# Performance work log

Measured on AMD Instinct MI355X. Metric: run time of the kernel, lower is better.

Reference implementation:

```python
import jax, jax.numpy as jnp
import numpy as np

# alphas = cfg.model.mmd.alphas ** k for k in range(-3, 2), base = 2.0
ALPHAS = tuple(2.0 ** k for k in range(-3, 2))


def _sq_dist(x, y):
    # x: (..., n, c), y: (..., m, c) -> (..., n, m) squared euclidean distance
    xx = jnp.sum(x * x, axis=-1)[..., :, None]
    yy = jnp.sum(y * y, axis=-1)[..., None, :]
    xy = jnp.einsum('...ic,...jc->...ij', x, y)
    return jnp.maximum(xx + yy - 2.0 * xy, 0.0)


def _multi_gauss(d2):
    # sum over alphas of exp(-alpha * dist^2); d2 is already the squared distance
    return sum(jnp.exp(-a * d2) for a in ALPHAS)


def setup_inputs() -> dict:
    key = jax.random.key(0)
    k1, k2, k3, k4 = jax.random.split(key, 4)
    b, ns, nq, ng, nsf, nqf, c = 8, 5, 75, 4, 49, 49, 64
    support_xf = jax.random.normal(k1, (b, ns, ng, nsf, c), dtype=jnp.float32)
    query_xf = jax.random.normal(k2, (b, nq, ng, nqf, c), dtype=jnp.float32)
    beta = jax.random.uniform(k3, (b, nq, ns, ng, nsf), dtype=jnp.float32)
    gamma = jax.random.uniform(k4, (b, nq, ns, ng, nqf), dtype=jnp.float32)
    return {"support_xf": support_xf, "query_xf": query_xf, "beta": beta, "gamma": gamma}


def reference(support_xf, query_xf, beta, gamma):
    # support_xf: (b, ns, ng, nsf, c); query_xf: (b, nq, ng, nqf, c)
    # beta, gamma: (b, nq, ns, ng, nsf/nqf)
    Kss = _multi_gauss(_sq_dist(support_xf, support_xf))   # (b, ns, ng, nsf, nsf)
    Kqq = _multi_gauss(_sq_dist(query_xf, query_xf))       # (b, nq, ng, nqf, nqf)

    # cross squared distances: (b, nq, ns, ng, nsf, nqf)
    s_sq = jnp.sum(support_xf * support_xf, axis=-1)        # (b, ns, ng, nsf)
    q_sq = jnp.sum(query_xf * query_xf, axis=-1)            # (b, nq, ng, nqf)
    sq_dot = jnp.einsum('bsgic,bvgjc->bvsgij', support_xf, query_xf)
    d2_sq = jnp.maximum(
        s_sq[:, None, :, :, :, None] + q_sq[:, :, None, :, None, :] - 2.0 * sq_dot, 0.0)
    Ksq = _multi_gauss(d2_sq)                               # (b, nq, ns, ng, nsf, nqf)

    # beta^T Kss beta  (Kss broadcast over the query axis)
    mmd_s = jnp.einsum('bvsgi,bsgij,bvsgj->bvsg', beta, Kss, beta)
    # gamma^T Kqq gamma (Kqq broadcast over the support axis)
    mmd_q = jnp.einsum('bvsgi,bvgij,bvsgj->bvsg', gamma, Kqq, gamma)
    # beta^T Ksq gamma
    mmd_sq = jnp.einsum('bvsgi,bvsgij,bvsgj->bvsg', beta, Ksq, gamma)

    mmd_dis = mmd_s + mmd_q - 2.0 * mmd_sq                  # (b, nq, ns, ng)
    return jnp.mean(mmd_dis, axis=-1)                       # (b, nq, ns)
```

## Files before the change

### kernel.cpp

```cpp
#include <hip/hip_runtime.h>

#define BB 8
#define NS 5
#define NQ 75
#define NG 4
#define NF 49
#define CDIM 64

#define SUP2 8192
#define NOUT (BB * NQ * NS)
#define NFORM (BB * NG * NS)
#define NCROSS (BB * NQ * NG * 2)

typedef __attribute__((ext_vector_type(8))) short bf16x8;
typedef __attribute__((ext_vector_type(16))) float f32x16;

__device__ __forceinline__ float multi_gauss(float d2) {
    d2 = fmaxf(d2, 0.f);
    float e  = __expf(-0.125f * d2);
    float e2 = e * e, e4 = e2 * e2, e8 = e4 * e4, e16 = e8 * e8;
    return e + e2 + e4 + e8 + e16;
}
__device__ __forceinline__ float multi_gauss2(float arg) {
    float e  = __builtin_amdgcn_exp2f(arg);
    float e2 = e * e, e4 = e2 * e2, e8 = e4 * e4, e16 = e8 * e8;
    return ((e + e2) + (e4 + e8)) + e16;
}
__device__ __forceinline__ unsigned short f2bf(float x) {
    union { float f; unsigned u; } c; c.f = x;
    unsigned r = c.u + 0x7FFFu + ((c.u >> 16) & 1u);
    return (unsigned short)(r >> 16);
}
__device__ __forceinline__ float bf2f(unsigned short h) {
    union { float f; unsigned u; } c; c.u = ((unsigned)h) << 16; return c.f;
}
__device__ __forceinline__ unsigned pack2bf(float x, float y) {
    return (__float_as_uint(x) >> 16) | (__float_as_uint(y) & 0xffff0000u);
}
__device__ __forceinline__ float wred(float x) {
    for (int o = 32; o; o >>= 1) x += __shfl_down(x, o, 64);
    return x;
}

__global__ __launch_bounds__(256) void prep(
    const float* __restrict__ sup,
    unsigned short* __restrict__ whi, float* __restrict__ wssq,
    float* __restrict__ out)
{
    int idx = blockIdx.x * 256 + threadIdx.x;
    if (idx < NOUT) out[idx] = 0.f;

    int row = idx >> 4, c4 = idx & 15;
    int bg = row >> 8, p = row & 255;
    int b = bg >> 2, g = bg & 3;
    int s = p / 49, i = p - s * 49;
    const float* src = (p < 245)
        ? sup + ((size_t)(((b * NS + s) * NG + g) * NF + i)) * CDIM + c4 * 4 : nullptr;

    float4 x = make_float4(0.f, 0.f, 0.f, 0.f);
    if (src) x = *(const float4*)src;
    ushort4 h4;
    h4.x = f2bf(x.x); h4.y = f2bf(x.y); h4.z = f2bf(x.z); h4.w = f2bf(x.w);
    ((ushort4*)whi)[idx] = h4;
    float v2 = x.x * x.x + x.y * x.y + x.z * x.z + x.w * x.w;
    v2 += __shfl_down(v2, 8, 64);
    v2 += __shfl_down(v2, 4, 64);
    v2 += __shfl_down(v2, 2, 64);
    v2 += __shfl_down(v2, 1, 64);
    if ((idx & 15) == 0) wssq[row] = v2;
}

__global__ __launch_bounds__(256, 5) void mmd_main(
    const unsigned short* __restrict__ whi, const float* __restrict__ wssq,
    const float* __restrict__ sup, const float* __restrict__ qry,
    const float* __restrict__ beta, const float* __restrict__ gamma,
    float* __restrict__ out)
{
    __shared__ __align__(16) union {
        struct {
            union {
                unsigned short Q[64 * 72];
                float kq[2 * 32 * 33];
            } qu;
            float ssqQ[64];
            float ssqS[256];
            float sbetaP[256];
            float sgam[NS][64];
            float red_sq[NS], red_qq[NS];
        } c;
        struct {
            unsigned short A[64 * 72];
            unsigned short Bt[32 * 72];
            float fssq[64];
            float red_s[96];
        } f;
    } sm;

    int blk = blockIdx.x;
    int t = threadIdx.x;
    int w = t >> 6, lane = t & 63, lrow = lane & 31, lhalf = lane >> 5;
    const bf16x8* W = (const bf16x8*)whi;
    const float c2  = -0.18033688f;
    const float k2c =  0.36067376f;

    if (blk >= NFORM) {
        int cc = blk - NFORM;
        int h = cc & 1;
        int g = (cc >> 1) & 3;
        int v = (cc >> 3) % NQ;
        int b = cc / (NQ * NG * 2);
        int qc = h * 32;
        int srow0 = (b * NG + g) * 256;

        const int cMTS[4] = {1, 3, 4, 6};
        const int cMTP[4] = {0, 2, 5, 7};
        int mtS = cMTS[w], mtP = cMTP[w];

        for (int u = t; u < 512; u += 256) {
            int row = u >> 3, c8 = u & 7;
            float4 x0 = make_float4(0.f, 0.f, 0.f, 0.f), x1 = x0;
            if (row < NF) {
                const float4* qp = (const float4*)
                    (qry + ((size_t)(((b * NQ + v) * NG + g) * NF + row)) * CDIM + c8 * 8);
                x0 = qp[0]; x1 = qp[1];
            }
            uint4 pk;
            pk.x = pack2bf(x0.x, x0.y);
            pk.y = pack2bf(x0.z, x0.w);
            pk.z = pack2bf(x1.x, x1.y);
            pk.w = pack2bf(x1.z, x1.w);
            *(uint4*)&sm.c.qu.Q[row * 72 + c8 * 8] = pk;
            float v2 = x0.x * x0.x + x0.y * x0.y + x0.z * x0.z + x0.w * x0.w
                     + x1.x * x1.x + x1.y * x1.y + x1.z * x1.z + x1.w * x1.w;
            v2 += __shfl_down(v2, 4, 64);
            v2 += __shfl_down(v2, 2, 64);
            v2 += __shfl_down(v2, 1, 64);
            if ((u & 7) == 0) sm.c.ssqQ[row] = v2;
        }
        {
            int p = t;
            sm.c.ssqS[p] = wssq[srow0 + p];
            int s = p / 49, i = p - s * 49;
            sm.c.sbetaP[p] = (p < 245)
                ? beta[(size_t)(((b * NQ + v) * NS + s) * NG + g) * NF + i] : 0.f;
            for (int u = t; u < NS * 64; u += 256) {
                int s2 = u >> 6, i2 = u & 63;
                sm.c.sgam[s2][i2] = (i2 < NF)
                    ? gamma[(size_t)(((b * NQ + v) * NS + s2) * NG + g) * NF + i2] : 0.f;
            }
            if (t < NS) { sm.c.red_sq[t] = 0.f; sm.c.red_qq[t] = 0.f; }
        }
        __syncthreads();

        f32x16 acc[3];
#pragma unroll
        for (int mi = 0; mi < 3; ++mi)
#pragma unroll
            for (int q = 0; q < 16; ++q) acc[mi][q] = 0.f;

        const unsigned short* Qs = sm.c.qu.Q;
#pragma unroll
        for (int kc = 0; kc < 4; ++kc) {
            int ko = kc * 2 + lhalf;
            int qoff = kc * 16 + lhalf * 8;
            bf16x8 bh = *(const bf16x8*)&Qs[(qc + lrow) * 72 + qoff];
            bf16x8 a0 = W[(srow0 + mtS * 32 + lrow) * 8 + ko];
            bf16x8 a1 = W[(srow0 + mtP * 32 + lrow) * 8 + ko];
            acc[0] = __builtin_amdgcn_mfma_f32_32x32x16_bf16(a0, bh, acc[0], 0, 0, 0);
            acc[1] = __builtin_amdgcn_mfma_f32_32x32x16_bf16(a1, bh, acc[1], 0, 0, 0);
            if (w >= 2) {
                bf16x8 a2 = *(const bf16x8*)&Qs[((w - 2) * 32 + lrow) * 72 + qoff];
                acc[2] = __builtin_amdgcn_mfma_f32_32x32x16_bf16(a2, bh, acc[2], 0, 0, 0);
            }
        }
        __syncthreads();

        if (w >= 2) {
            float* kq = sm.c.qu.kq;
            int base = (w - 2) * 1056 + lrow;
#pragma unroll
            for (int reg = 0; reg < 16; ++reg) {
                int r32 = (reg & 3) + 8 * (reg >> 2) + 4 * lhalf;
                kq[base + r32 * 33] = acc[2][reg];
            }
        }

        float qsq = sm.c.ssqQ[qc + lrow];
        float c2q = c2 * qsq;

        float tsA, tsB;
        {
            int s_lo = (mtS * 32) / 49;
            int bnd = (s_lo + 1) * 49;
            float tA = 0.f, tB = 0.f;
#pragma unroll
            for (int grp = 0; grp < 4; ++grp) {
                int rbase = mtS * 32 + grp * 8 + 4 * lhalf;
                float4 sqv = *(const float4*)&sm.c.ssqS[rbase];
                float4 bvv = *(const float4*)&sm.c.sbetaP[rbase];
#pragma unroll
                for (int q = 0; q < 4; ++q) {
                    float sq = (q == 0) ? sqv.x : (q == 1) ? sqv.y : (q == 2) ? sqv.z : sqv.w;
                    float bv = (q == 0) ? bvv.x : (q == 1) ? bvv.y : (q == 2) ? bvv.z : bvv.w;
                    float arg = fmaf(k2c, acc[0][grp * 4 + q], fmaf(c2, sq, c2q));
                    float con = bv * multi_gauss2(arg);
                    bool lo = (rbase + q) < bnd;
                    tA += lo ? con : 0.f;
                    tB += lo ? 0.f : con;
                }
            }
            tsA = tA; tsB = tB;
        }
        float tsP;
        {
            float tP = 0.f;
#pragma unroll
            for (int grp = 0; grp < 4; ++grp) {
                int rbase = mtP * 32 + grp * 8 + 4 * lhalf;
                float4 sqv = *(const float4*)&sm.c.ssqS[rbase];
                float4 bvv = *(const float4*)&sm.c.sbetaP[rbase];
#pragma unroll
                for (int q = 0; q < 4; ++q) {
                    float sq = (q == 0) ? sqv.x : (q == 1) ? sqv.y : (q == 2) ? sqv.z : sqv.w;
                    float bv = (q == 0) ? bvv.x : (q == 1) ? bvv.y : (q == 2) ? bvv.z : bvv.w;
                    float arg = fmaf(k2c, acc[1][grp * 4 + q], fmaf(c2, sq, c2q));
                    tP = fmaf(bv, multi_gauss2(arg), tP);
                }
            }
            tsP = tP;
        }
        {
            int s_lo = (mtS * 32) / 49;
            int s_hi = s_lo + 1;
            int sP = (mtP * 32) / 49;
            float rA = wred(tsA * sm.c.sgam[s_lo][qc + lrow]);
            float rB = wred(tsB * sm.c.sgam[s_hi][qc + lrow]);
            float rP = wred(tsP * sm.c.sgam[sP][qc + lrow]);
            if (lane == 0) {
                atomicAdd(&sm.c.red_sq[s_lo], rA);
                atomicAdd(&sm.c.red_sq[s_hi], rB);
                atomicAdd(&sm.c.red_sq[sP], rP);
            }
        }
        __syncthreads();

        {
            int colg = qc + lrow;
            const float* kq = sm.c.qu.kq;
            float gq[NS];
#pragma unroll
            for (int s = 0; s < NS; ++s) gq[s] = sm.c.sgam[s][colg];
            float qs[NS] = {0.f, 0.f, 0.f, 0.f, 0.f};
#pragma unroll
            for (int gg = 0; gg < 2; ++gg) {
                int rb = w * 16 + lhalf * 8 + gg * 4;
                float4 sqv = *(const float4*)&sm.c.ssqQ[rb];
                float kvv[4];
#pragma unroll
                for (int q = 0; q < 4; ++q) {
                    int row = rb + q;
                    float dot = kq[(row >> 5) * 1056 + (row & 31) * 33 + lrow];
                    float sq = (q == 0) ? sqv.x : (q == 1) ? sqv.y : (q == 2) ? sqv.z : sqv.w;
                    float arg = fmaf(k2c, dot, fmaf(c2, sq, c2q));
                    kvv[q] = (row == colg) ? 5.0f : multi_gauss2(arg);
                }
#pragma unroll
                for (int s = 0; s < NS; ++s) {
                    float4 gi = *(const float4*)&sm.c.sgam[s][rb];
                    qs[s] = fmaf(gi.x, kvv[0], qs[s]);
                    qs[s] = fmaf(gi.y, kvv[1], qs[s]);
                    qs[s] = fmaf(gi.z, kvv[2], qs[s]);
                    qs[s] = fmaf(gi.w, kvv[3], qs[s]);
                }
            }
#pragma unroll
            for (int s = 0; s < NS; ++s) {
                float r = wred(qs[s] * gq[s]);
                if (lane == 0) atomicAdd(&sm.c.red_qq[s], r);
            }
        }
        __syncthreads();
        if (t < NS)
            atomicAdd(&out[((size_t)b * NQ + v) * NS + t],
                      0.25f * sm.c.red_qq[t] - 0.5f * sm.c.red_sq[t]);
    } else {
        int k = blk;
        int s = k % NS;
        int bg = k / NS;
        int g = bg & 3, b = bg >> 2;

        if (t < 96) sm.f.red_s[t] = 0.f;

        for (int u = t; u < 1024; u += 256) {
            int i = u >> 4, c4 = u & 15;
            float4 x = make_float4(0.f, 0.f, 0.f, 0.f);
            if (i < NF)
                x = *(const float4*)(sup + ((size_t)(((b * NS + s) * NG + g) * NF + i)) * CDIM + c4 * 4);
            ushort4 h4;
            h4.x = f2bf(x.x); h4.y = f2bf(x.y); h4.z = f2bf(x.z); h4.w = f2bf(x.w);
            *(ushort4*)&sm.f.A[i * 72 + c4 * 4] = h4;
            float v2 = x.x * x.x + x.y * x.y + x.z * x.z + x.w * x.w;
            v2 += __shfl_down(v2, 8, 64);
            v2 += __shfl_down(v2, 4, 64);
            v2 += __shfl_down(v2, 2, 64);
            v2 += __shfl_down(v2, 1, 64);
            if ((u & 15) == 0) sm.f.fssq[i] = v2;
        }
        __syncthreads();

        int mt = w >> 1, nt = w & 1;
        f32x16 acc;
#pragma unroll
        for (int q = 0; q < 16; ++q) acc[q] = 0.f;
#pragma unroll
        for (int kc = 0; kc < 4; ++kc) {
            int ko = kc * 2 + lhalf;
            bf16x8 a  = *(const bf16x8*)&sm.f.A[(mt * 32 + lrow) * 72 + ko * 8];
            bf16x8 bb = *(const bf16x8*)&sm.f.A[(nt * 32 + lrow) * 72 + ko * 8];
            acc = __builtin_amdgcn_mfma_f32_32x32x16_bf16(a, bb, acc, 0, 0, 0);
        }
        __syncthreads();

        int cj = nt * 32 + lrow;
        float sqj = sm.f.fssq[cj];
#pragma unroll
        for (int reg = 0; reg < 16; ++reg) {
            int ri = mt * 32 + (reg & 3) + 8 * (reg >> 2) + 4 * lhalf;
            float kv = (ri == cj) ? 5.0f : multi_gauss(sm.f.fssq[ri] + sqj - 2.f * acc[reg]);
            sm.f.A[ri * 72 + cj] = f2bf(kv);
        }

        for (int pass = 0; pass < 3; ++pass) {
            __syncthreads();
            for (int u = t; u < 2048; u += 256) {
                int v32 = u >> 6, j = u & 63;
                int v = pass * 32 + v32;
                unsigned short val = 0;
                if (v < NQ && j < NF)
                    val = f2bf(beta[(size_t)(((b * NQ + v) * NS + s) * NG + g) * NF + j]);
                sm.f.Bt[v32 * 72 + j] = val;
            }
            __syncthreads();
            if (w < 2) {
                int m = w;
                f32x16 yacc;
#pragma unroll
                for (int q = 0; q < 16; ++q) yacc[q] = 0.f;
#pragma unroll
                for (int kc = 0; kc < 4; ++kc) {
                    int ko = kc * 2 + lhalf;
                    bf16x8 af = *(const bf16x8*)&sm.f.A[(m * 32 + lrow) * 72 + ko * 8];
                    bf16x8 bf = *(const bf16x8*)&sm.f.Bt[lrow * 72 + ko * 8];
                    yacc = __builtin_amdgcn_mfma_f32_32x32x16_bf16(af, bf, yacc, 0, 0, 0);
                }
                float p = 0.f;
#pragma unroll
                for (int reg = 0; reg < 16; ++reg) {
                    int i = m * 32 + (reg & 3) + 8 * (reg >> 2) + 4 * lhalf;
                    p = fmaf(yacc[reg], bf2f(sm.f.Bt[lrow * 72 + i]), p);
                }
                p += __shfl_xor(p, 32, 64);
                if (lane < 32) atomicAdd(&sm.f.red_s[pass * 32 + lrow], p);
            }
        }
        __syncthreads();
        if (t < NQ)
            atomicAdd(&out[((size_t)b * NQ + t) * NS + s], 0.25f * sm.f.red_s[t]);
    }
}

extern "C" void kernel_launch(void* const* d_in, const int* in_sizes, int n_in,
                              void* d_out, int out_size, void* d_ws, size_t ws_size,
                              hipStream_t stream) {
    const float* sup   = (const float*)d_in[0];
    const float* qry   = (const float*)d_in[1];
    const float* beta  = (const float*)d_in[2];
    const float* gamma = (const float*)d_in[3];
    float* out = (float*)d_out;

    unsigned short* whi = (unsigned short*)d_ws;
    float* wssq = (float*)(whi + (size_t)SUP2 * 64);

    prep<<<(SUP2 * 16) / 256, 256, 0, stream>>>(sup, whi, wssq, out);
    mmd_main<<<NFORM + NCROSS, 256, 0, stream>>>(whi, wssq, sup, qry, beta, gamma, out);
}
```

Before: 120.8 us.

## Merge query-column halves into one 512-thread block per cross tile

Each cross-term block now covers both 32-column halves of the query features, using 512 threads (two groups of four waves) instead of two 256-thread blocks. The query tile, gamma, beta and support norms are loaded into shared memory once per (b,v,g) rather than twice, and the shared Kqq dot buffer doubles to hold both halves. Formation blocks also run at 512 threads, but only four waves do the MFMA and kernel-evaluation work. This cuts redundant global loads and block count, at the cost of larger blocks, a bigger shared footprint and idle waves in the formation path.

```diff
diff --git a/kernel.cpp b/kernel.cpp
--- a/kernel.cpp
+++ b/kernel.cpp
@@ -10,7 +10,7 @@
 #define SUP2 8192
 #define NOUT (BB * NQ * NS)
 #define NFORM (BB * NG * NS)
-#define NCROSS (BB * NQ * NG * 2)
+#define NCROSS (BB * NQ * NG)
 
 typedef __attribute__((ext_vector_type(8))) short bf16x8;
 typedef __attribute__((ext_vector_type(16))) float f32x16;
@@ -70,7 +70,7 @@
     if ((idx & 15) == 0) wssq[row] = v2;
 }
 
-__global__ __launch_bounds__(256, 5) void mmd_main(
+__global__ __launch_bounds__(512, 4) void mmd_main(
     const unsigned short* __restrict__ whi, const float* __restrict__ wssq,
     const float* __restrict__ sup, const float* __restrict__ qry,
     const float* __restrict__ beta, const float* __restrict__ gamma,
@@ -80,7 +80,7 @@
         struct {
             union {
                 unsigned short Q[64 * 72];
-                float kq[2 * 32 * 33];
+                float kq[4 * 32 * 33];
             } qu;
             float ssqQ[64];
             float ssqS[256];
@@ -105,19 +105,19 @@
 
     if (blk >= NFORM) {
         int cc = blk - NFORM;
-        int h = cc & 1;
-        int g = (cc >> 1) & 3;
-        int v = (cc >> 3) % NQ;
-        int b = cc / (NQ * NG * 2);
+        int g = cc & 3;
+        int v = (cc >> 2) % NQ;
+        int b = cc / (NQ * NG);
+        int srow0 = (b * NG + g) * 256;
+        int h = w >> 2, w4 = w & 3;
         int qc = h * 32;
-        int srow0 = (b * NG + g) * 256;
 
         const int cMTS[4] = {1, 3, 4, 6};
         const int cMTP[4] = {0, 2, 5, 7};
-        int mtS = cMTS[w], mtP = cMTP[w];
-
-        for (int u = t; u < 512; u += 256) {
-            int row = u >> 3, c8 = u & 7;
+        int mtS = cMTS[w4], mtP = cMTP[w4];
+
+        {
+            int row = t >> 3, c8 = t & 7;
             float4 x0 = make_float4(0.f, 0.f, 0.f, 0.f), x1 = x0;
             if (row < NF) {
                 const float4* qp = (const float4*)
@@ -135,21 +135,21 @@
             v2 += __shfl_down(v2, 4, 64);
             v2 += __shfl_down(v2, 2, 64);
             v2 += __shfl_down(v2, 1, 64);
-            if ((u & 7) == 0) sm.c.ssqQ[row] = v2;
-        }
-        {
+            if ((t & 7) == 0) sm.c.ssqQ[row] = v2;
+        }
+        if (t < 256) {
             int p = t;
             sm.c.ssqS[p] = wssq[srow0 + p];
             int s = p / 49, i = p - s * 49;
             sm.c.sbetaP[p] = (p < 245)
                 ? beta[(size_t)(((b * NQ + v) * NS + s) * NG + g) * NF + i] : 0.f;
-            for (int u = t; u < NS * 64; u += 256) {
-                int s2 = u >> 6, i2 = u & 63;
-                sm.c.sgam[s2][i2] = (i2 < NF)
-                    ? gamma[(size_t)(((b * NQ + v) * NS + s2) * NG + g) * NF + i2] : 0.f;
-            }
-            if (t < NS) { sm.c.red_sq[t] = 0.f; sm.c.red_qq[t] = 0.f; }
-        }
+        }
+        if (t < NS * 64) {
+            int s2 = t >> 6, i2 = t & 63;
+            sm.c.sgam[s2][i2] = (i2 < NF)
+                ? gamma[(size_t)(((b * NQ + v) * NS + s2) * NG + g) * NF + i2] : 0.f;
+        }
+        if (t < NS) { sm.c.red_sq[t] = 0.f; sm.c.red_qq[t] = 0.f; }
         __syncthreads();
 
         f32x16 acc[3];
@@ -168,16 +168,16 @@
             bf16x8 a1 = W[(srow0 + mtP * 32 + lrow) * 8 + ko];
             acc[0] = __builtin_amdgcn_mfma_f32_32x32x16_bf16(a0, bh, acc[0], 0, 0, 0);
             acc[1] = __builtin_amdgcn_mfma_f32_32x32x16_bf16(a1, bh, acc[1], 0, 0, 0);
-            if (w >= 2) {
-                bf16x8 a2 = *(const bf16x8*)&Qs[((w - 2) * 32 + lrow) * 72 + qoff];
+            if (w4 >= 2) {
+                bf16x8 a2 = *(const bf16x8*)&Qs[((w4 - 2) * 32 + lrow) * 72 + qoff];
                 acc[2] = __builtin_amdgcn_mfma_f32_32x32x16_bf16(a2, bh, acc[2], 0, 0, 0);
             }
         }
         __syncthreads();
 
-        if (w >= 2) {
+        if (w4 >= 2) {
             float* kq = sm.c.qu.kq;
-            int base = (w - 2) * 1056 + lrow;
+            int base = (h * 2 + (w4 - 2)) * 1056 + lrow;
 #pragma unroll
             for (int reg = 0; reg < 16; ++reg) {
                 int r32 = (reg & 3) + 8 * (reg >> 2) + 4 * lhalf;
@@ -253,13 +253,13 @@
             float qs[NS] = {0.f, 0.f, 0.f, 0.f, 0.f};
 #pragma unroll
             for (int gg = 0; gg < 2; ++gg) {
-                int rb = w * 16 + lhalf * 8 + gg * 4;
+                int rb = w4 * 16 + lhalf * 8 + gg * 4;
                 float4 sqv = *(const float4*)&sm.c.ssqQ[rb];
                 float kvv[4];
 #pragma unroll
                 for (int q = 0; q < 4; ++q) {
                     int row = rb + q;
-                    float dot = kq[(row >> 5) * 1056 + (row & 31) * 33 + lrow];
+                    float dot = kq[(h * 2 + (row >> 5)) * 1056 + (row & 31) * 33 + lrow];
                     float sq = (q == 0) ? sqv.x : (q == 1) ? sqv.y : (q == 2) ? sqv.z : sqv.w;
                     float arg = fmaf(k2c, dot, fmaf(c2, sq, c2q));
                     kvv[q] = (row == colg) ? 5.0f : multi_gauss2(arg);
@@ -291,7 +291,7 @@
 
         if (t < 96) sm.f.red_s[t] = 0.f;
 
-        for (int u = t; u < 1024; u += 256) {
+        for (int u = t; u < 1024; u += 512) {
             int i = u >> 4, c4 = u & 15;
             float4 x = make_float4(0.f, 0.f, 0.f, 0.f);
             if (i < NF)
@@ -308,31 +308,35 @@
         }
         __syncthreads();
 
-        int mt = w >> 1, nt = w & 1;
         f32x16 acc;
 #pragma unroll
         for (int q = 0; q < 16; ++q) acc[q] = 0.f;
-#pragma unroll
-        for (int kc = 0; kc < 4; ++kc) {
-            int ko = kc * 2 + lhalf;
-            bf16x8 a  = *(const bf16x8*)&sm.f.A[(mt * 32 + lrow) * 72 + ko * 8];
-            bf16x8 bb = *(const bf16x8*)&sm.f.A[(nt * 32 + lrow) * 72 + ko * 8];
-            acc = __builtin_amdgcn_mfma_f32_32x32x16_bf16(a, bb, acc, 0, 0, 0);
-        }
-        __syncthreads();
-
-        int cj = nt * 32 + lrow;
-        float sqj = sm.f.fssq[cj];
-#pragma unroll
-        for (int reg = 0; reg < 16; ++reg) {
-            int ri = mt * 32 + (reg & 3) + 8 * (reg >> 2) + 4 * lhalf;
-            float kv = (ri == cj) ? 5.0f : multi_gauss(sm.f.fssq[ri] + sqj - 2.f * acc[reg]);
-            sm.f.A[ri * 72 + cj] = f2bf(kv);
+        int mt = (w >> 1) & 1, nt = w & 1;
+        if (w < 4) {
+#pragma unroll
+            for (int kc = 0; kc < 4; ++kc) {
+                int ko = kc * 2 + lhalf;
+                bf16x8 a  = *(const bf16x8*)&sm.f.A[(mt * 32 + lrow) * 72 + ko * 8];
+                bf16x8 bb = *(const bf16x8*)&sm.f.A[(nt * 32 + lrow) * 72 + ko * 8];
+                acc = __builtin_amdgcn_mfma_f32_32x32x16_bf16(a, bb, acc, 0, 0, 0);
+            }
+        }
+        __syncthreads();
+
+        if (w < 4) {
+            int cj = nt * 32 + lrow;
+            float sqj = sm.f.fssq[cj];
+#pragma unroll
+            for (int reg = 0; reg < 16; ++reg) {
+                int ri = mt * 32 + (reg & 3) + 8 * (reg >> 2) + 4 * lhalf;
+                float kv = (ri == cj) ? 5.0f : multi_gauss(sm.f.fssq[ri] + sqj - 2.f * acc[reg]);
+                sm.f.A[ri * 72 + cj] = f2bf(kv);
+            }
         }
 
         for (int pass = 0; pass < 3; ++pass) {
             __syncthreads();
-            for (int u = t; u < 2048; u += 256) {
+            for (int u = t; u < 2048; u += 512) {
                 int v32 = u >> 6, j = u & 63;
                 int v = pass * 32 + v32;
                 unsigned short val = 0;
@@ -382,5 +386,5 @@
     float* wssq = (float*)(whi + (size_t)SUP2 * 64);
 
     prep<<<(SUP2 * 16) / 256, 256, 0, stream>>>(sup, whi, wssq, out);
-    mmd_main<<<NFORM + NCROSS, 256, 0, stream>>>(whi, wssq, sup, qry, beta, gamma, out);
-}
+    mmd_main<<<NFORM + NCROSS, 512, 0, stream>>>(whi, wssq, sup, qry, beta, gamma, out);
+}
```

Result: no change. 118.8 us (-1.6%).
